# Optimization experiments

Hardware: AMD Instinct MI355X
Metric: run time of the kernel (lower is better)

Reference implementation:

```python
import jax, jax.numpy as jnp
import numpy as np

B, S, H = 4, 512, 256

def setup_inputs() -> dict:
    key = jax.random.key(0)
    k1, k2, k3, k4 = jax.random.split(key, 4)
    scale = 1.0 / np.sqrt(H)
    return {
        "h": jax.random.normal(k1, (B, S, H), dtype=jnp.float32),
        "W_t": jax.random.normal(k2, (H, H), dtype=jnp.float32) * scale,
        "W_t_prime": jax.random.normal(k3, (H, H), dtype=jnp.float32) * scale,
        "b_h": jnp.zeros((H,), dtype=jnp.float32),
        "W_a": jax.random.normal(k4, (H,), dtype=jnp.float32) * scale,
        "b_a": jnp.zeros((), dtype=jnp.float32),
    }

def reference(h, W_t, W_t_prime, b_h, W_a, b_a):
    # Project once per timestep, then broadcast-add over the (t, t') pair grid.
    ht = jnp.einsum("bsh,hk->bsk", h, W_t)          # W_t applied to h^t
    htp = jnp.einsum("bsh,hk->bsk", h, W_t_prime)   # W_{t'} applied to h^{t'}
    # transformed: (B, S_t, S_t', H)
    transformed = ht[:, :, None, :] + htp[:, None, :, :] + b_h
    tanh_out = jnp.tanh(transformed)
    scores = jnp.einsum("bsth,h->bst", tanh_out, W_a) + b_a  # (B, S, S)
    scores = jax.nn.sigmoid(scores)
    attention_weights = jax.nn.softmax(scores, axis=2)
    output = jnp.einsum("bst,bth->bsh", attention_weights, h)
    return output, attention_weights
```

## Files before the change

kernel.cpp:

```cpp
#include <hip/hip_runtime.h>

#define Bn 4
#define Sn 512
#define Hn 256

#define CC   2.8853900817779268f
#define L2E  1.4426950408889634f

typedef __attribute__((ext_vector_type(4))) float f32x4;
typedef __attribute__((ext_vector_type(8))) short short8;

__device__ __forceinline__ unsigned short bf16rn(float f) {
    unsigned int u = __float_as_uint(f);
    u += 0x7fffu + ((u >> 16) & 1u);
    return (unsigned short)(u >> 16);
}
__device__ __forceinline__ float bf16tof(unsigned short b) {
    return __uint_as_float(((unsigned int)b) << 16);
}

__global__ __launch_bounds__(256) void prep_kernel(
    const float* __restrict__ h,  const float* __restrict__ Wt,
    const float* __restrict__ Wp, const float* __restrict__ Wa,
    const float* __restrict__ ba,
    unsigned short* __restrict__ h1, unsigned short* __restrict__ h2,
    unsigned short* __restrict__ wtp,
    float* __restrict__ wa2, float* __restrict__ cst)
{
    __shared__ float tile[64 * 68];
    __shared__ float red4[4];
    const int tid = threadIdx.x;
    const int bid = blockIdx.x;

    if (bid < 256) {
        const int base = (bid * 256 + tid) * 8;
        float4 v0 = *(const float4*)&h[base];
        float4 v1 = *(const float4*)&h[base + 4];
        float f[8] = {v0.x, v0.y, v0.z, v0.w, v1.x, v1.y, v1.z, v1.w};
        unsigned short b1[8], b2[8];
#pragma unroll
        for (int i = 0; i < 8; i++) {
            b1[i] = bf16rn(f[i]);
            b2[i] = bf16rn(f[i] - bf16tof(b1[i]));
        }
        uint4 u1, u2;
        u1.x = (unsigned)b1[0] | ((unsigned)b1[1] << 16);
        u1.y = (unsigned)b1[2] | ((unsigned)b1[3] << 16);
        u1.z = (unsigned)b1[4] | ((unsigned)b1[5] << 16);
        u1.w = (unsigned)b1[6] | ((unsigned)b1[7] << 16);
        u2.x = (unsigned)b2[0] | ((unsigned)b2[1] << 16);
        u2.y = (unsigned)b2[2] | ((unsigned)b2[3] << 16);
        u2.z = (unsigned)b2[4] | ((unsigned)b2[5] << 16);
        u2.w = (unsigned)b2[6] | ((unsigned)b2[7] << 16);
        *(uint4*)&h1[base] = u1;
        *(uint4*)&h2[base] = u2;

        if (bid == 0) {
            float w = Wa[tid];
#pragma unroll
            for (int off = 32; off >= 1; off >>= 1) w += __shfl_xor(w, off, 64);
            if ((tid & 63) == 0) red4[tid >> 6] = w;
            __syncthreads();
            wa2[tid] = -2.0f * Wa[tid];
            if (tid == 0)
                cst[0] = -L2E * ((red4[0] + red4[1] + red4[2] + red4[3]) + ba[0]);
        }
    } else {
        const int sb  = bid - 256;
        const int mat = sb >> 4;
        const int t4  = sb & 15;
        const int k0  = (t4 >> 2) * 64, n0 = (t4 & 3) * 64;
        const float* __restrict__ W = mat ? Wp : Wt;

#pragma unroll
        for (int i = 0; i < 4; i++) {
            const int idx = tid + 256 * i;
            const int kr = idx >> 4, nq = idx & 15;
            *(float4*)&tile[kr * 68 + nq * 4] =
                *(const float4*)&W[(k0 + kr) * Hn + n0 + nq * 4];
        }
        __syncthreads();

        unsigned short* p1 = wtp + mat * 2 * 65536;
        unsigned short* p2 = p1 + 65536;
#pragma unroll
        for (int i = 0; i < 8; i++) {
            const int idx = tid + 256 * i;
            const int n = idx >> 5, kp = idx & 31;
            const float f0 = tile[(2 * kp) * 68 + n];
            const float f1 = tile[(2 * kp + 1) * 68 + n];
            const unsigned short a0 = bf16rn(f0), a1 = bf16rn(f1);
            const unsigned short c0 = bf16rn(f0 - bf16tof(a0));
            const unsigned short c1 = bf16rn(f1 - bf16tof(a1));
            const int dw = ((n0 + n) * 256 + k0) / 2 + kp;
            ((unsigned int*)p1)[dw] = (unsigned)a0 | ((unsigned)a1 << 16);
            ((unsigned int*)p2)[dw] = (unsigned)c0 | ((unsigned)c1 << 16);
        }
    }
}

__global__ __launch_bounds__(256) void gemm_kernel(
    const unsigned short* __restrict__ h1, const unsigned short* __restrict__ h2,
    const unsigned short* __restrict__ wtp, const float* __restrict__ bh,
    float* __restrict__ Egt, float* __restrict__ Egp4)
{
    __shared__ char lds[20480];

    const int tid = threadIdx.x;
    const int mb = blockIdx.x >> 3;
    const int nb = blockIdx.x & 7;
    const int m0 = mb * 64;
    const bool isT = (nb < 4);
    const int n0l = isT ? nb * 64 : (nb - 4) * 64;
    const unsigned short* pB1 = wtp + (isT ? 0 : 2 * 65536);
    const unsigned short* pB2 = pB1 + 65536;

    const int w    = tid >> 6;
    const int lane = tid & 63;
    const int quad = lane >> 4;
    const int l15  = lane & 15;

    f32x4 acc[4];
#pragma unroll
    for (int i = 0; i < 4; i++) acc[i] = (f32x4){0.f, 0.f, 0.f, 0.f};

    const int ssel = tid >> 7;
    const int spl  = (tid >> 6) & 1;
    const int srow = (tid & 63) >> 2;
    const int sseg = tid & 3;
    const unsigned short* gsrc =
        (ssel == 0) ? (spl ? h2 : h1) : (spl ? pB2 : pB1);
    const int growbase = (ssel == 0) ? m0 : n0l;
    char* ldsdst = lds + (ssel * 2 + spl) * 5120;

    for (int ks = 0; ks < 256; ks += 32) {
        __syncthreads();
#pragma unroll
        for (int i = 0; i < 4; i++) {
            const int row = srow + i * 16;
            uint4 v = *(const uint4*)&gsrc[(growbase + row) * 256 + ks + sseg * 8];
            *(uint4*)(ldsdst + row * 80 + sseg * 16) = v;
        }
        __syncthreads();

        const char* Ab = lds;
        const char* Bb = lds + 10240;
        const short8 b1 = *(const short8*)(Bb + (w * 16 + l15) * 80 + quad * 16);
        const short8 b2 = *(const short8*)(Bb + 5120 + (w * 16 + l15) * 80 + quad * 16);
#pragma unroll
        for (int mt = 0; mt < 4; mt++) {
            const short8 a1 = *(const short8*)(Ab + (mt * 16 + l15) * 80 + quad * 16);
            const short8 a2 = *(const short8*)(Ab + 5120 + (mt * 16 + l15) * 80 + quad * 16);
            acc[mt] = __builtin_amdgcn_mfma_f32_16x16x32_bf16(a1, b1, acc[mt], 0, 0, 0);
            acc[mt] = __builtin_amdgcn_mfma_f32_16x16x32_bf16(a1, b2, acc[mt], 0, 0, 0);
            acc[mt] = __builtin_amdgcn_mfma_f32_16x16x32_bf16(a2, b1, acc[mt], 0, 0, 0);
        }
    }

    __syncthreads();
    float* ct = (float*)lds;
#pragma unroll
    for (int mt = 0; mt < 4; mt++)
#pragma unroll
        for (int r = 0; r < 4; r++)
            ct[(mt * 16 + quad * 4 + r) * 68 + w * 16 + l15] = acc[mt][r];
    __syncthreads();

    const int b  = m0 >> 9;
    const int s0 = m0 & 511;
    if (isT) {
        const int n0g = nb * 64;
#pragma unroll
        for (int i = 0; i < 4; i++) {
            const int item = tid + i * 256;
            const int mr = item >> 4, nq = item & 15;
            const float4 c  = *(const float4*)&ct[mr * 68 + nq * 4];
            const float4 bv = *(const float4*)&bh[n0g + nq * 4];
            float4 o;
            o.x = __builtin_amdgcn_exp2f((c.x + bv.x) * CC);
            o.y = __builtin_amdgcn_exp2f((c.y + bv.y) * CC);
            o.z = __builtin_amdgcn_exp2f((c.z + bv.z) * CC);
            o.w = __builtin_amdgcn_exp2f((c.w + bv.w) * CC);
            *(float4*)&Egt[(m0 + mr) * Hn + n0g + nq * 4] = o;
        }
    } else {
        const int kq0 = (nb - 4) * 16;
#pragma unroll
        for (int i = 0; i < 4; i++) {
            const int item = tid + i * 256;
            const int mr = item & 63, nq = item >> 6;
            const float4 c = *(const float4*)&ct[mr * 68 + nq * 4];
            float4 o;
            o.x = __builtin_amdgcn_exp2f(c.x * CC);
            o.y = __builtin_amdgcn_exp2f(c.y * CC);
            o.z = __builtin_amdgcn_exp2f(c.z * CC);
            o.w = __builtin_amdgcn_exp2f(c.w * CC);
            *(float4*)&Egp4[b * 131072 + (kq0 + nq) * 2048 + (s0 + mr) * 4] = o;
        }
    }
}

__global__ __launch_bounds__(1024) void attn_kernel(
    const float* __restrict__ hsrc, const float* __restrict__ Egt,
    const float* __restrict__ Egp4, const float* __restrict__ wa2,
    const float* __restrict__ cst,
    float* __restrict__ out, float* __restrict__ out_attn)
{
    __shared__ char smem[40960];
    float*  attn_l = (float*)smem;
    float*  accl   = (float*)(smem + 8192);
    float*  red    = (float*)(smem + 16384);
    float4* part   = (float4*)(smem + 8192);

    const int tid = threadIdx.x;
    const int tp  = tid & 511;
    const int kh  = tid >> 9;
    const int b   = blockIdx.x & 3;
    const int t0  = (blockIdx.x >> 2) << 2;

    const int kbu = __builtin_amdgcn_readfirstlane(kh << 5);

    const float* __restrict__ egt = Egt + (b * Sn + t0) * Hn;
    const float4* __restrict__ ep = (const float4*)(Egp4 + b * (Hn * Sn));

    float acc[4] = {0.f, 0.f, 0.f, 0.f};

    float4 w4c  = *(const float4*)&wa2[kbu * 4];
    float4 eg0c = *(const float4*)&egt[0 * Hn + kbu * 4];
    float4 eg1c = *(const float4*)&egt[1 * Hn + kbu * 4];
    float4 eg2c = *(const float4*)&egt[2 * Hn + kbu * 4];
    float4 eg3c = *(const float4*)&egt[3 * Hn + kbu * 4];

#pragma unroll 2
    for (int kk = 0; kk < 32; kk++) {
        const int k4n = kbu + ((kk + 1) & 31);
        const float4 w4n  = *(const float4*)&wa2[k4n * 4];
        const float4 eg0n = *(const float4*)&egt[0 * Hn + k4n * 4];
        const float4 eg1n = *(const float4*)&egt[1 * Hn + k4n * 4];
        const float4 eg2n = *(const float4*)&egt[2 * Hn + k4n * 4];
        const float4 eg3n = *(const float4*)&egt[3 * Hn + k4n * 4];

        const float4 cur = ep[(kbu + kk) * Sn + tp];

        const float4 egs[4] = {eg0c, eg1c, eg2c, eg3c};
#pragma unroll
        for (int r = 0; r < 4; r++) {
            const float4 eg = egs[r];
            const float d1 = fmaf(cur.x, eg.x, 1.0f);
            const float d2 = fmaf(cur.y, eg.y, 1.0f);
            const float d3 = fmaf(cur.z, eg.z, 1.0f);
            const float d4 = fmaf(cur.w, eg.w, 1.0f);
            const float p12 = d1 * d2, p34 = d3 * d4;
            const float n12 = fmaf(w4c.x, d2, w4c.y * d1);
            const float n34 = fmaf(w4c.z, d4, w4c.w * d3);
            const float num = fmaf(n12, p34, n34 * p12);
            acc[r] = fmaf(num, __builtin_amdgcn_rcpf(p12 * p34), acc[r]);
        }

        w4c = w4n; eg0c = eg0n; eg1c = eg1n; eg2c = eg2n; eg3c = eg3n;
    }

    if (kh == 1) {
#pragma unroll
        for (int r = 0; r < 4; r++) accl[r * 512 + tp] = acc[r];
    }
    __syncthreads();

    float ex[4];
    const float k0 = cst[0];
    if (kh == 0) {
#pragma unroll
        for (int r = 0; r < 4; r++) {
            const float a   = acc[r] + accl[r * 512 + tp];
            const float e1  = __builtin_amdgcn_exp2f(fmaf(-L2E, a, k0));
            const float sig = __builtin_amdgcn_rcpf(1.0f + e1);
            ex[r] = __builtin_amdgcn_exp2f(L2E * sig);
        }
        const int lane = tid & 63, wid = tid >> 6;
#pragma unroll
        for (int r = 0; r < 4; r++) {
            float v = ex[r];
#pragma unroll
            for (int off = 32; off >= 1; off >>= 1) v += __shfl_xor(v, off, 64);
            if (lane == 0) red[r * 8 + wid] = v;
        }
    }
    __syncthreads();

    if (kh == 0) {
#pragma unroll
        for (int r = 0; r < 4; r++) {
            float tot = 0.f;
#pragma unroll
            for (int i = 0; i < 8; i++) tot += red[r * 8 + i];
            const float a = ex[r] * __builtin_amdgcn_rcpf(tot);
            attn_l[r * Sn + tp] = a;
            out_attn[(b * Sn + t0 + r) * Sn + tp] = a;
        }
    }
    __syncthreads();

    const int c4 = tid & 63;
    const int q  = tid >> 6;

    const float* __restrict__ hb = hsrc + (b * Sn + q * 32) * Hn + c4 * 4;

    float4 a4[4];
#pragma unroll
    for (int r = 0; r < 4; r++) a4[r] = (float4){0.f, 0.f, 0.f, 0.f};

#pragma unroll 2
    for (int j4 = 0; j4 < 8; j4++) {
        float4 wv[4];
#pragma unroll
        for (int r = 0; r < 4; r++)
            wv[r] = *(const float4*)&attn_l[r * Sn + q * 32 + j4 * 4];
#pragma unroll
        for (int i = 0; i < 4; i++) {
            const float4 hv = *(const float4*)&hb[(j4 * 4 + i) * Hn];
#pragma unroll
            for (int r = 0; r < 4; r++) {
                const float wr = ((const float*)&wv[r])[i];
                a4[r].x = fmaf(wr, hv.x, a4[r].x);
                a4[r].y = fmaf(wr, hv.y, a4[r].y);
                a4[r].z = fmaf(wr, hv.z, a4[r].z);
                a4[r].w = fmaf(wr, hv.w, a4[r].w);
            }
        }
    }
    __syncthreads();

    if (q < 8) {
#pragma unroll
        for (int r = 0; r < 4; r++) part[(q * 4 + r) * 64 + c4] = a4[r];
    }
    __syncthreads();
    if (q >= 8) {
#pragma unroll
        for (int r = 0; r < 4; r++) {
            float4 p = part[((q - 8) * 4 + r) * 64 + c4];
            p.x += a4[r].x; p.y += a4[r].y; p.z += a4[r].z; p.w += a4[r].w;
            part[((q - 8) * 4 + r) * 64 + c4] = p;
        }
    }
    __syncthreads();

    {
        const int col = tid & 255;
        const int r   = tid >> 8;
        const float* pf = (const float*)part;
        float s = 0.f;
#pragma unroll
        for (int qq = 0; qq < 8; qq++)
            s += pf[((qq * 4 + r) * 64 + (col >> 2)) * 4 + (col & 3)];
        out[(b * Sn + t0 + r) * Hn + col] = s;
    }
}

extern "C" void kernel_launch(void* const* d_in, const int* in_sizes, int n_in,
                              void* d_out, int out_size, void* d_ws, size_t ws_size,
                              hipStream_t stream) {
    const float* h   = (const float*)d_in[0];
    const float* Wt  = (const float*)d_in[1];
    const float* Wtp = (const float*)d_in[2];
    const float* bh  = (const float*)d_in[3];
    const float* Wa  = (const float*)d_in[4];
    const float* ba  = (const float*)d_in[5];

    float* out      = (float*)d_out;
    float* out_attn = out + Bn * Sn * Hn;

    float* ws   = (float*)d_ws;
    float* Egt  = ws;
    float* Egp4 = ws + 524288;
    float* wa2  = ws + 1048576;
    float* cst  = ws + 1048832;
    unsigned short* h1  = (unsigned short*)(ws + 1048840);
    unsigned short* h2  = h1 + 2048 * 256;
    unsigned short* wtp = h2 + 2048 * 256;

    prep_kernel<<<dim3(288), dim3(256), 0, stream>>>(
        h, Wt, Wtp, Wa, ba, h1, h2, wtp, wa2, cst);
    gemm_kernel<<<dim3(256), dim3(256), 0, stream>>>(h1, h2, wtp, bh, Egt, Egp4);
    attn_kernel<<<dim3(Bn * (Sn / 4)), dim3(1024), 0, stream>>>(
        h, Egt, Egp4, wa2, cst, out, out_attn);
}
```

Measured before the change: 116.4 us.

## Fuse bf16 split-conversion prep into GEMM kernel, staging full K in LDS

Removes the separate prep kernel by having each GEMM block convert its 64-row h tile and its 64-column W tile to hi/lo bf16 directly into LDS, holding the full K=256 extent. This drops one kernel launch and the global round-trip of the converted h and W arrays. In exchange, W is converted redundantly by every block that uses it. The roughly 150KB LDS footprint also limits occupancy to one block per CU.

Result: no change. 114.3 us (-1.8%).

```diff
diff --git a/kernel.cpp b/kernel.cpp
--- a/kernel.cpp
+++ b/kernel.cpp
@@ -19,59 +19,66 @@
     return __uint_as_float(((unsigned int)b) << 16);
 }
 
-__global__ __launch_bounds__(256) void prep_kernel(
+__global__ __launch_bounds__(256) void gemm_kernel(
     const float* __restrict__ h,  const float* __restrict__ Wt,
     const float* __restrict__ Wp, const float* __restrict__ Wa,
-    const float* __restrict__ ba,
-    unsigned short* __restrict__ h1, unsigned short* __restrict__ h2,
-    unsigned short* __restrict__ wtp,
+    const float* __restrict__ ba, const float* __restrict__ bh,
+    float* __restrict__ Egt, float* __restrict__ Egp4,
     float* __restrict__ wa2, float* __restrict__ cst)
 {
-    __shared__ float tile[64 * 68];
-    __shared__ float red4[4];
+    __shared__ char lds[152640];
+    unsigned short* A1 = (unsigned short*)lds;
+    unsigned short* A2 = (unsigned short*)(lds + 33792);
+    unsigned short* B1 = (unsigned short*)(lds + 67584);
+    unsigned short* B2 = (unsigned short*)(lds + 101376);
+    float* tile = (float*)(lds + 135168);
+    float* red4 = (float*)(lds + 152576);
+
     const int tid = threadIdx.x;
-    const int bid = blockIdx.x;
-
-    if (bid < 256) {
-        const int base = (bid * 256 + tid) * 8;
-        float4 v0 = *(const float4*)&h[base];
-        float4 v1 = *(const float4*)&h[base + 4];
-        float f[8] = {v0.x, v0.y, v0.z, v0.w, v1.x, v1.y, v1.z, v1.w};
-        unsigned short b1[8], b2[8];
-#pragma unroll
-        for (int i = 0; i < 8; i++) {
-            b1[i] = bf16rn(f[i]);
-            b2[i] = bf16rn(f[i] - bf16tof(b1[i]));
-        }
-        uint4 u1, u2;
-        u1.x = (unsigned)b1[0] | ((unsigned)b1[1] << 16);
-        u1.y = (unsigned)b1[2] | ((unsigned)b1[3] << 16);
-        u1.z = (unsigned)b1[4] | ((unsigned)b1[5] << 16);
-        u1.w = (unsigned)b1[6] | ((unsigned)b1[7] << 16);
-        u2.x = (unsigned)b2[0] | ((unsigned)b2[1] << 16);
-        u2.y = (unsigned)b2[2] | ((unsigned)b2[3] << 16);
-        u2.z = (unsigned)b2[4] | ((unsigned)b2[5] << 16);
-        u2.w = (unsigned)b2[6] | ((unsigned)b2[7] << 16);
-        *(uint4*)&h1[base] = u1;
-        *(uint4*)&h2[base] = u2;
-
-        if (bid == 0) {
-            float w = Wa[tid];
-#pragma unroll
-            for (int off = 32; off >= 1; off >>= 1) w += __shfl_xor(w, off, 64);
-            if ((tid & 63) == 0) red4[tid >> 6] = w;
-            __syncthreads();
-            wa2[tid] = -2.0f * Wa[tid];
-            if (tid == 0)
-                cst[0] = -L2E * ((red4[0] + red4[1] + red4[2] + red4[3]) + ba[0]);
-        }
-    } else {
-        const int sb  = bid - 256;
-        const int mat = sb >> 4;
-        const int t4  = sb & 15;
-        const int k0  = (t4 >> 2) * 64, n0 = (t4 & 3) * 64;
-        const float* __restrict__ W = mat ? Wp : Wt;
-
+    const int mb  = blockIdx.x >> 3;
+    const int nb  = blockIdx.x & 7;
+    const int m0  = mb * 64;
+    const bool isT = (nb < 4);
+    const int n0  = (isT ? nb : nb - 4) * 64;
+    const float* __restrict__ W = isT ? Wt : Wp;
+
+    if (blockIdx.x == 0) {
+        float wv = Wa[tid];
+#pragma unroll
+        for (int off = 32; off >= 1; off >>= 1) wv += __shfl_xor(wv, off, 64);
+        if ((tid & 63) == 0) red4[tid >> 6] = wv;
+        __syncthreads();
+        wa2[tid] = -2.0f * Wa[tid];
+        if (tid == 0)
+            cst[0] = -L2E * ((red4[0] + red4[1] + red4[2] + red4[3]) + ba[0]);
+    }
+
+    {
+        const int row = tid >> 2;
+        const int seg = (tid & 3) * 64;
+        const float* __restrict__ src = h + (m0 + row) * Hn + seg;
+        unsigned int* d1 = (unsigned int*)A1 + (row * 264 + seg) / 2;
+        unsigned int* d2 = (unsigned int*)A2 + (row * 264 + seg) / 2;
+#pragma unroll
+        for (int i = 0; i < 16; i++) {
+            const float4 v = ((const float4*)src)[i];
+            const float f[4] = {v.x, v.y, v.z, v.w};
+            unsigned short b1[4], b2[4];
+#pragma unroll
+            for (int j = 0; j < 4; j++) {
+                b1[j] = bf16rn(f[j]);
+                b2[j] = bf16rn(f[j] - bf16tof(b1[j]));
+            }
+            d1[2 * i]     = (unsigned)b1[0] | ((unsigned)b1[1] << 16);
+            d1[2 * i + 1] = (unsigned)b1[2] | ((unsigned)b1[3] << 16);
+            d2[2 * i]     = (unsigned)b2[0] | ((unsigned)b2[1] << 16);
+            d2[2 * i + 1] = (unsigned)b2[2] | ((unsigned)b2[3] << 16);
+        }
+    }
+
+    for (int kt = 0; kt < 4; kt++) {
+        const int k0 = kt * 64;
+        __syncthreads();
 #pragma unroll
         for (int i = 0; i < 4; i++) {
             const int idx = tid + 256 * i;
@@ -80,9 +87,6 @@
                 *(const float4*)&W[(k0 + kr) * Hn + n0 + nq * 4];
         }
         __syncthreads();
-
-        unsigned short* p1 = wtp + mat * 2 * 65536;
-        unsigned short* p2 = p1 + 65536;
 #pragma unroll
         for (int i = 0; i < 8; i++) {
             const int idx = tid + 256 * i;
@@ -92,28 +96,13 @@
             const unsigned short a0 = bf16rn(f0), a1 = bf16rn(f1);
             const unsigned short c0 = bf16rn(f0 - bf16tof(a0));
             const unsigned short c1 = bf16rn(f1 - bf16tof(a1));
-            const int dw = ((n0 + n) * 256 + k0) / 2 + kp;
-            ((unsigned int*)p1)[dw] = (unsigned)a0 | ((unsigned)a1 << 16);
-            ((unsigned int*)p2)[dw] = (unsigned)c0 | ((unsigned)c1 << 16);
-        }
-    }
-}
-
-__global__ __launch_bounds__(256) void gemm_kernel(
-    const unsigned short* __restrict__ h1, const unsigned short* __restrict__ h2,
-    const unsigned short* __restrict__ wtp, const float* __restrict__ bh,
-    float* __restrict__ Egt, float* __restrict__ Egp4)
-{
-    __shared__ char lds[20480];
-
-    const int tid = threadIdx.x;
-    const int mb = blockIdx.x >> 3;
-    const int nb = blockIdx.x & 7;
-    const int m0 = mb * 64;
-    const bool isT = (nb < 4);
-    const int n0l = isT ? nb * 64 : (nb - 4) * 64;
-    const unsigned short* pB1 = wtp + (isT ? 0 : 2 * 65536);
-    const unsigned short* pB2 = pB1 + 65536;
+            ((unsigned int*)B1)[n * 132 + k0 / 2 + kp] =
+                (unsigned)a0 | ((unsigned)a1 << 16);
+            ((unsigned int*)B2)[n * 132 + k0 / 2 + kp] =
+                (unsigned)c0 | ((unsigned)c1 << 16);
+        }
+    }
+    __syncthreads();
 
     const int w    = tid >> 6;
     const int lane = tid & 63;
@@ -124,33 +113,16 @@
 #pragma unroll
     for (int i = 0; i < 4; i++) acc[i] = (f32x4){0.f, 0.f, 0.f, 0.f};
 
-    const int ssel = tid >> 7;
-    const int spl  = (tid >> 6) & 1;
-    const int srow = (tid & 63) >> 2;
-    const int sseg = tid & 3;
-    const unsigned short* gsrc =
-        (ssel == 0) ? (spl ? h2 : h1) : (spl ? pB2 : pB1);
-    const int growbase = (ssel == 0) ? m0 : n0l;
-    char* ldsdst = lds + (ssel * 2 + spl) * 5120;
-
+#pragma unroll 2
     for (int ks = 0; ks < 256; ks += 32) {
-        __syncthreads();
-#pragma unroll
-        for (int i = 0; i < 4; i++) {
-            const int row = srow + i * 16;
-            uint4 v = *(const uint4*)&gsrc[(growbase + row) * 256 + ks + sseg * 8];
-            *(uint4*)(ldsdst + row * 80 + sseg * 16) = v;
-        }
-        __syncthreads();
-
-        const char* Ab = lds;
-        const char* Bb = lds + 10240;
-        const short8 b1 = *(const short8*)(Bb + (w * 16 + l15) * 80 + quad * 16);
-        const short8 b2 = *(const short8*)(Bb + 5120 + (w * 16 + l15) * 80 + quad * 16);
+        const int bof = (w * 16 + l15) * 264 + ks + quad * 8;
+        const short8 b1 = *(const short8*)(B1 + bof);
+        const short8 b2 = *(const short8*)(B2 + bof);
 #pragma unroll
         for (int mt = 0; mt < 4; mt++) {
-            const short8 a1 = *(const short8*)(Ab + (mt * 16 + l15) * 80 + quad * 16);
-            const short8 a2 = *(const short8*)(Ab + 5120 + (mt * 16 + l15) * 80 + quad * 16);
+            const int aof = (mt * 16 + l15) * 264 + ks + quad * 8;
+            const short8 a1 = *(const short8*)(A1 + aof);
+            const short8 a2 = *(const short8*)(A2 + aof);
             acc[mt] = __builtin_amdgcn_mfma_f32_16x16x32_bf16(a1, b1, acc[mt], 0, 0, 0);
             acc[mt] = __builtin_amdgcn_mfma_f32_16x16x32_bf16(a1, b2, acc[mt], 0, 0, 0);
             acc[mt] = __builtin_amdgcn_mfma_f32_16x16x32_bf16(a2, b1, acc[mt], 0, 0, 0);
@@ -158,7 +130,7 @@
     }
 
     __syncthreads();
-    float* ct = (float*)lds;
+    float* ct = tile;
 #pragma unroll
     for (int mt = 0; mt < 4; mt++)
 #pragma unroll
@@ -375,13 +347,9 @@
     float* Egp4 = ws + 524288;
     float* wa2  = ws + 1048576;
     float* cst  = ws + 1048832;
-    unsigned short* h1  = (unsigned short*)(ws + 1048840);
-    unsigned short* h2  = h1 + 2048 * 256;
-    unsigned short* wtp = h2 + 2048 * 256;
-
-    prep_kernel<<<dim3(288), dim3(256), 0, stream>>>(
-        h, Wt, Wtp, Wa, ba, h1, h2, wtp, wa2, cst);
-    gemm_kernel<<<dim3(256), dim3(256), 0, stream>>>(h1, h2, wtp, bh, Egt, Egp4);
+
+    gemm_kernel<<<dim3(256), dim3(256), 0, stream>>>(
+        h, Wt, Wtp, Wa, ba, bh, Egt, Egp4, wa2, cst);
     attn_kernel<<<dim3(Bn * (Sn / 4)), dim3(1024), 0, stream>>>(
         h, Egt, Egp4, wa2, cst, out, out_attn);
 }
```
